# Kernel tuning notes

Measured on AMD Instinct MI355X. Metric: run time of the kernel, lower is better.

## Reference

```python
import jax, jax.numpy as jnp
import numpy as np

P = 100   # num_proxies
N = 1024  # num_samples
D = 512


def _edge_index():
    # complete bipartite proxy<->sample graph, both directions, plus self-loops
    # (PyG GATConv adds self-loops for all nodes by default)
    p = np.arange(P)
    s = np.arange(P, P + N)
    src_ps = np.repeat(p, N)   # proxy -> sample
    dst_ps = np.tile(s, P)
    loops = np.arange(P + N)
    src = np.concatenate([src_ps, dst_ps, loops]).astype(np.int32)
    dst = np.concatenate([dst_ps, src_ps, loops]).astype(np.int32)
    return jnp.asarray(src), jnp.asarray(dst)


def setup_inputs() -> dict:
    key = jax.random.key(0)
    ks = jax.random.split(key, 10)
    sc = 1.0 / np.sqrt(D)
    src, dst = _edge_index()
    return {
        "x": jax.random.normal(ks[0], (N, D), jnp.float32),
        "proxies": jax.random.normal(ks[1], (P, D), jnp.float32),
        "W1": jax.random.normal(ks[2], (D, D), jnp.float32) * sc,
        "a_src1": jax.random.normal(ks[3], (D,), jnp.float32) * sc,
        "a_dst1": jax.random.normal(ks[4], (D,), jnp.float32) * sc,
        "b1": jnp.zeros((D,), jnp.float32),
        "W2": jax.random.normal(ks[5], (D, D), jnp.float32) * sc,
        "a_src2": jax.random.normal(ks[6], (D,), jnp.float32) * sc,
        "a_dst2": jax.random.normal(ks[7], (D,), jnp.float32) * sc,
        "b2": jnp.zeros((D,), jnp.float32),
        "fc_w": jax.random.normal(ks[8], (D, 100), jnp.float32) * sc,
        "fc_b": jnp.zeros((100,), jnp.float32),
        "src": src,
        "dst": dst,
    }


def _gat_conv(x, src, dst, W, a_src, a_dst, b, n_nodes):
    # PyG GATConv, heads=1, concat=True, negative_slope=0.2
    h = x @ W                      # [n, D]
    l_src = h @ a_src              # [n]
    l_dst = h @ a_dst              # [n]
    e = jax.nn.leaky_relu(l_src[src] + l_dst[dst], 0.2)   # [E]
    # segment softmax over edges sharing the same destination
    e = e - jax.ops.segment_max(e, dst, num_segments=n_nodes)[dst]
    ex = jnp.exp(e)
    denom = jax.ops.segment_sum(ex, dst, num_segments=n_nodes)[dst]
    alpha = ex / denom             # [E]
    out = jax.ops.segment_sum(alpha[:, None] * h[src], dst, num_segments=n_nodes)
    return out + b


def reference(x, proxies, W1, a_src1, a_dst1, b1, W2, a_src2, a_dst2, b2, fc_w, fc_b, src, dst):
    n = P + N
    h = jnp.concatenate([proxies, x], axis=0)          # [P+N, D]
    h = jax.nn.relu(_gat_conv(h, src, dst, W1, a_src1, a_dst1, b1, n))
    # Dropout -> identity (eval)
    h = jax.nn.relu(_gat_conv(h, src, dst, W2, a_src2, a_dst2, b2, n))
    preds = h @ fc_w + fc_b                            # [P+N, 100]
    return preds[P:], h[P:]
```

## Files before the change

### kernel.cpp

```cpp
#include <hip/hip_runtime.h>

#define PP 100
#define NS 1024
#define NN 1124
#define DD 512
#define CC 100
#define NTHR 256

typedef _Float16 f16;
typedef _Float16 f16x8 __attribute__((ext_vector_type(8)));
typedef float    f32x4 __attribute__((ext_vector_type(4)));

__device__ __forceinline__ float lk(float v) { return v > 0.f ? v : 0.2f * v; }
__device__ __forceinline__ f16 hif(float v) { return (f16)v; }
__device__ __forceinline__ f16 lof(float v) { return (f16)(v - (float)((f16)v)); }

__device__ __forceinline__ void mgemm_core(
    const f16* __restrict__ Ah, const f16* __restrict__ Al,
    const f16* __restrict__ Bth, const f16* __restrict__ Btl,
    int K, int row0, int col0, f16* __restrict__ lds, f32x4 acc[2][2])
{
  const int t = threadIdx.x;
  const int lane = t & 63, w = t >> 6;
  const int wr = w >> 1, wc = w & 1;
  f16* Ash = lds;
  f16* Asl = lds + 2560;
  f16* Bsh = lds + 5120;
  f16* Bsl = lds + 7680;
  const int srow = t >> 2, su = t & 3;
  const size_t aoff = (size_t)(row0 + srow) * K + su * 8;
  const size_t boff = (size_t)(col0 + srow) * K + su * 8;
  const int lw = srow * 40 + su * 8;
  f32x4 pa0 = *(const f32x4*)(Ah + aoff);
  f32x4 pa1 = *(const f32x4*)(Al + aoff);
  f32x4 pb0 = *(const f32x4*)(Bth + boff);
  f32x4 pb1 = *(const f32x4*)(Btl + boff);
  const int fra = wr * 32 + (lane & 15);
  const int frb = wc * 32 + (lane & 15);
  const int fu  = (lane >> 4) * 8;
  for (int kt = 32; kt <= K; kt += 32) {
    *(f32x4*)(Ash + lw) = pa0;
    *(f32x4*)(Asl + lw) = pa1;
    *(f32x4*)(Bsh + lw) = pb0;
    *(f32x4*)(Bsl + lw) = pb1;
    __syncthreads();
    if (kt < K) {
      pa0 = *(const f32x4*)(Ah + aoff + kt);
      pa1 = *(const f32x4*)(Al + aoff + kt);
      pb0 = *(const f32x4*)(Bth + boff + kt);
      pb1 = *(const f32x4*)(Btl + boff + kt);
    }
    f16x8 ah[2], al[2], bh[2], bl[2];
#pragma unroll
    for (int m = 0; m < 2; ++m) {
      ah[m] = *(const f16x8*)(Ash + (fra + m * 16) * 40 + fu);
      al[m] = *(const f16x8*)(Asl + (fra + m * 16) * 40 + fu);
    }
#pragma unroll
    for (int n = 0; n < 2; ++n) {
      bh[n] = *(const f16x8*)(Bsh + (frb + n * 16) * 40 + fu);
      bl[n] = *(const f16x8*)(Bsl + (frb + n * 16) * 40 + fu);
    }
#pragma unroll
    for (int m = 0; m < 2; ++m)
#pragma unroll
      for (int n = 0; n < 2; ++n) {
        acc[m][n] = __builtin_amdgcn_mfma_f32_16x16x32_f16(ah[m], bh[n], acc[m][n], 0, 0, 0);
        acc[m][n] = __builtin_amdgcn_mfma_f32_16x16x32_f16(al[m], bh[n], acc[m][n], 0, 0, 0);
        acc[m][n] = __builtin_amdgcn_mfma_f32_16x16x32_f16(ah[m], bl[n], acc[m][n], 0, 0, 0);
      }
    __syncthreads();
  }
}


__device__ __forceinline__ void cvt_tile(
    const float* __restrict__ in, int R, int Cin,
    f16* __restrict__ oh, f16* __restrict__ ol, int ldo,
    int ti, int tj, f16 (*th)[72], f16 (*tl)[72])
{
  const int t = threadIdx.x;
#pragma unroll
  for (int p = 0; p < 4; ++p) {
    const int f = t + p * 256;
    const int i = f >> 4, j4 = (f & 15) * 4;
    const int gi = ti * 64 + i, gj = tj * 64 + j4;
    float4 v = make_float4(0.f, 0.f, 0.f, 0.f);
    if (gi < R && gj + 3 < Cin) v = *(const float4*)(in + (size_t)gi * Cin + gj);
    th[i][j4 + 0] = hif(v.x); tl[i][j4 + 0] = lof(v.x);
    th[i][j4 + 1] = hif(v.y); tl[i][j4 + 1] = lof(v.y);
    th[i][j4 + 2] = hif(v.z); tl[i][j4 + 2] = lof(v.z);
    th[i][j4 + 3] = hif(v.w); tl[i][j4 + 3] = lof(v.w);
  }
  __syncthreads();
#pragma unroll
  for (int p = 0; p < 2; ++p) {
    const int f = t + p * 256;
    const int j = f >> 3, i8 = (f & 7) * 8;
    f16x8 vh, vl;
#pragma unroll
    for (int e = 0; e < 8; ++e) { vh[e] = th[i8 + e][j]; vl[e] = tl[i8 + e][j]; }
    const size_t o = (size_t)(tj * 64 + j) * ldo + ti * 64 + i8;
    *(f16x8*)(oh + o) = vh;
    *(f16x8*)(ol + o) = vl;
  }
}

__global__ __launch_bounds__(NTHR) void prep_k(
    const float* __restrict__ x, const float* __restrict__ prox,
    const float* __restrict__ W1, const float* __restrict__ W2,
    const float* __restrict__ fcw,
    const float* __restrict__ as1, const float* __restrict__ ad1,
    const float* __restrict__ as2, const float* __restrict__ ad2,
    f16* xth, f16* xtl, f16* pth, f16* ptl,
    f16* W1th, f16* W1tl, f16* W2th, f16* W2tl, f16* fwth, f16* fwtl,
    float* v1s, float* v1d, float* v2s, float* v2d)
{
  __shared__ f16 th[64][72];
  __shared__ f16 tl[64][72];
  const int b = blockIdx.x;
  if (b < 64) {
    cvt_tile(W1, 512, 512, W1th, W1tl, 512, b >> 3, b & 7, th, tl);
  } else if (b < 128) {
    cvt_tile(W2, 512, 512, W2th, W2tl, 512, (b - 64) >> 3, (b - 64) & 7, th, tl);
  } else if (b < 256) {
    cvt_tile(x, NS, 512, xth, xtl, NS, (b - 128) >> 3, (b - 128) & 7, th, tl);
  } else if (b < 272) {
    cvt_tile(prox, PP, 512, pth, ptl, 128, (b - 256) >> 3, (b - 256) & 7, th, tl);
  } else if (b < 288) {
    cvt_tile(fcw, 512, CC, fwth, fwtl, 512, (b - 272) >> 1, (b - 272) & 1, th, tl);
  } else {
    const int wid  = (b - 288) * 4 + (threadIdx.x >> 6);
    const int lane = threadIdx.x & 63;
    const int r = wid & 511;
    const bool l1 = (wid < 512);
    const float* W = l1 ? W1 : W2;
    const float4* a4 = (const float4*)(l1 ? as1 : as2);
    const float4* b4 = (const float4*)(l1 ? ad1 : ad2);
    const float4* w4 = (const float4*)(W + (size_t)r * DD);
    float4 w0 = w4[lane], w1 = w4[lane + 64];
    float4 a0 = a4[lane], a1 = a4[lane + 64];
    float4 b0 = b4[lane], b1 = b4[lane + 64];
    float s1 = w0.x * a0.x + w0.y * a0.y + w0.z * a0.z + w0.w * a0.w
             + w1.x * a1.x + w1.y * a1.y + w1.z * a1.z + w1.w * a1.w;
    float s2 = w0.x * b0.x + w0.y * b0.y + w0.z * b0.z + w0.w * b0.w
             + w1.x * b1.x + w1.y * b1.y + w1.z * b1.z + w1.w * b1.w;
#pragma unroll
    for (int off = 32; off > 0; off >>= 1) {
      s1 += __shfl_down(s1, off);
      s2 += __shfl_down(s2, off);
    }
    if (lane == 0) {
      (l1 ? v1s : v2s)[r] = s1;
      (l1 ? v1d : v2d)[r] = s2;
    }
  }
}

__global__ __launch_bounds__(NTHR) void lvec_k(
    const float* __restrict__ A0, const float* __restrict__ A1, int split,
    const float* __restrict__ vs, const float* __restrict__ vd,
    float* __restrict__ ls, float* __restrict__ ld)
{
  const int r    = blockIdx.x * 4 + (threadIdx.x >> 6);
  const int lane = threadIdx.x & 63;
  if (r >= NN) return;
  const float* row = (r < split) ? A0 + (size_t)r * DD : A1 + (size_t)(r - split) * DD;
  const float4* r4 = (const float4*)row;
  const float4* s4 = (const float4*)vs;
  const float4* d4 = (const float4*)vd;
  float4 v0 = r4[lane], v1 = r4[lane + 64];
  float4 a0 = s4[lane], a1 = s4[lane + 64];
  float4 b0 = d4[lane], b1 = d4[lane + 64];
  float s1 = v0.x * a0.x + v0.y * a0.y + v0.z * a0.z + v0.w * a0.w
           + v1.x * a1.x + v1.y * a1.y + v1.z * a1.z + v1.w * a1.w;
  float s2 = v0.x * b0.x + v0.y * b0.y + v0.z * b0.z + v0.w * b0.w
           + v1.x * b1.x + v1.y * b1.y + v1.z * b1.z + v1.w * b1.w;
#pragma unroll
  for (int off = 32; off > 0; off >>= 1) {
    s1 += __shfl_down(s1, off);
    s2 += __shfl_down(s2, off);
  }
  if (lane == 0) { ls[r] = s1; ld[r] = s2; }
}

__global__ __launch_bounds__(NTHR) void alpha_k(
    const float* __restrict__ ls, const float* __restrict__ ld,
    f16* __restrict__ Esh, f16* __restrict__ Esl,
    float* __restrict__ esS, float* __restrict__ izS,
    f16* __restrict__ Eph, f16* __restrict__ Epl,
    float* __restrict__ esP, float* __restrict__ izP)
{
  const int t = threadIdx.x;
  if (blockIdx.x < 256) {
    const int lane = t & 63;
    const int i = blockIdx.x * 4 + (t >> 6);
    const float ldi = ld[PP + i];
    float e0 = lk(ls[lane] + ldi);
    float e1 = (lane < PP - 64) ? lk(ls[lane + 64] + ldi) : -1e30f;
    const float eself = lk(ls[PP + i] + ldi);
    float m = fmaxf(fmaxf(e0, e1), eself);
#pragma unroll
    for (int off = 1; off < 64; off <<= 1) m = fmaxf(m, __shfl_xor(m, off));
    float x0 = __expf(e0 - m);
    float x1 = (lane < PP - 64) ? __expf(e1 - m) : 0.f;
    float z = x0 + x1;
#pragma unroll
    for (int off = 1; off < 64; off <<= 1) z += __shfl_xor(z, off);
    Esh[(size_t)i * 128 + lane]      = hif(x0);
    Esl[(size_t)i * 128 + lane]      = lof(x0);
    Esh[(size_t)i * 128 + 64 + lane] = hif(x1);
    Esl[(size_t)i * 128 + 64 + lane] = lof(x1);
    if (lane == 0) {
      float xs = __expf(eself - m);
      esS[i] = xs;
      izS[i] = 1.f / (z + xs);
    }
  } else {
    const int i = blockIdx.x - 256;
    if (i >= PP) {
#pragma unroll
      for (int q = 0; q < 4; ++q) {
        Eph[(size_t)i * NS + t + q * 256] = (f16)0.f;
        Epl[(size_t)i * NS + t + q * 256] = (f16)0.f;
      }
      return;
    }
    __shared__ float red[4];
    const float ldi = ld[i];
    const float eself = lk(ls[i] + ldi);
    float e[4];
#pragma unroll
    for (int q = 0; q < 4; ++q) e[q] = lk(ls[PP + t + q * 256] + ldi);
    float m = fmaxf(fmaxf(fmaxf(e[0], e[1]), fmaxf(e[2], e[3])), eself);
#pragma unroll
    for (int off = 1; off < 64; off <<= 1) m = fmaxf(m, __shfl_xor(m, off));
    if ((t & 63) == 0) red[t >> 6] = m;
    __syncthreads();
    m = fmaxf(fmaxf(red[0], red[1]), fmaxf(red[2], red[3]));
    __syncthreads();
    float xq[4], z = 0.f;
#pragma unroll
    for (int q = 0; q < 4; ++q) { xq[q] = __expf(e[q] - m); z += xq[q]; }
#pragma unroll
    for (int off = 1; off < 64; off <<= 1) z += __shfl_xor(z, off);
    if ((t & 63) == 0) red[t >> 6] = z;
    __syncthreads();
#pragma unroll
    for (int q = 0; q < 4; ++q) {
      Eph[(size_t)i * NS + t + q * 256] = hif(xq[q]);
      Epl[(size_t)i * NS + t + q * 256] = lof(xq[q]);
    }
    if (t == 0) {
      float xs = __expf(eself - m);
      esP[i] = xs;
      izP[i] = 1.f / (red[0] + red[1] + red[2] + red[3] + xs);
    }
  }
}

__global__ __launch_bounds__(NTHR) void agg1_k(
    const f16* __restrict__ Es1h, const f16* __restrict__ Es1l,
    const f16* __restrict__ pth,  const f16* __restrict__ ptl,
    const f16* __restrict__ Eph,  const f16* __restrict__ Epl,
    const f16* __restrict__ xth,  const f16* __restrict__ xtl,
    const float* __restrict__ x, const float* __restrict__ prox,
    const float* __restrict__ esS, const float* __restrict__ izS,
    const float* __restrict__ esP, const float* __restrict__ izP,
    f16* __restrict__ M1h, f16* __restrict__ M1l)
{
  __shared__ __align__(16) f16 lds[10240];
  f32x4 acc[2][2] = {};
  const int t = threadIdx.x, lane = t & 63, w = t >> 6, wr = w >> 1, wc = w & 1;
  const int b = blockIdx.x;
  if (b < 128) {
    const int row0 = (b >> 3) * 64, col0 = (b & 7) * 64;
    mgemm_core(Es1h, Es1l, pth, ptl, 128, row0, col0, lds, acc);
#pragma unroll
    for (int m = 0; m < 2; ++m)
#pragma unroll
      for (int q = 0; q < 4; ++q) {
        const int r = row0 + wr * 32 + m * 16 + (lane >> 4) * 4 + q;
        const float e = esS[r], z = izS[r];
#pragma unroll
        for (int n = 0; n < 2; ++n) {
          const int c = col0 + wc * 32 + n * 16 + (lane & 15);
          const float v = (acc[m][n][q] + e * x[(size_t)r * DD + c]) * z;
          const size_t o = (size_t)(PP + r) * DD + c;
          M1h[o] = hif(v); M1l[o] = lof(v);
        }
      }
  } else {
    const int b2 = b - 128;
    const int row0 = (b2 >> 3) * 64, col0 = (b2 & 7) * 64;
    mgemm_core(Eph, Epl, xth, xtl, NS, row0, col0, lds, acc);
#pragma unroll
    for (int m = 0; m < 2; ++m)
#pragma unroll
      for (int q = 0; q < 4; ++q) {
        const int r = row0 + wr * 32 + m * 16 + (lane >> 4) * 4 + q;
        if (r < PP) {
          const float e = esP[r], z = izP[r];
#pragma unroll
          for (int n = 0; n < 2; ++n) {
            const int c = col0 + wc * 32 + n * 16 + (lane & 15);
            const float v = (acc[m][n][q] + e * prox[(size_t)r * DD + c]) * z;
            const size_t o = (size_t)r * DD + c;
            M1h[o] = hif(v); M1l[o] = lof(v);
          }
        }
      }
  }
}

__global__ __launch_bounds__(NTHR) void h1_k(
    const f16* __restrict__ M1h, const f16* __restrict__ M1l,
    const f16* __restrict__ W1th, const f16* __restrict__ W1tl,
    const float* __restrict__ b1, float* __restrict__ h1,
    f16* __restrict__ h1pth, f16* __restrict__ h1ptl)
{
  __shared__ __align__(16) f16 lds[10240];
  f32x4 acc[2][2] = {};
  const int t = threadIdx.x, lane = t & 63, w = t >> 6, wr = w >> 1, wc = w & 1;
  const int b = blockIdx.x;
  const int row0 = (b >> 3) * 64, col0 = (b & 7) * 64;
  mgemm_core(M1h, M1l, W1th, W1tl, DD, row0, col0, lds, acc);
#pragma unroll
  for (int m = 0; m < 2; ++m)
#pragma unroll
    for (int q = 0; q < 4; ++q) {
      const int r = row0 + wr * 32 + m * 16 + (lane >> 4) * 4 + q;
      if (r >= NN) continue;
#pragma unroll
      for (int n = 0; n < 2; ++n) {
        const int c = col0 + wc * 32 + n * 16 + (lane & 15);
        const float v = fmaxf(acc[m][n][q] + b1[c], 0.f);
        h1[(size_t)r * DD + c] = v;
        if (r < 128) {
          const size_t o = (size_t)c * 128 + r;
          f16 hh = (f16)0.f, ll = (f16)0.f;
          if (r < PP) { hh = hif(v); ll = lof(v); }
          h1pth[o] = hh; h1ptl[o] = ll;
        }
      }
    }
}

__global__ __launch_bounds__(NTHR) void agg2_k(
    const f16* __restrict__ Es2h, const f16* __restrict__ Es2l,
    const f16* __restrict__ h1pth, const f16* __restrict__ h1ptl,
    const float* __restrict__ h1,
    const float* __restrict__ esS, const float* __restrict__ izS,
    f16* __restrict__ M2h, f16* __restrict__ M2l)
{
  __shared__ __align__(16) f16 lds[10240];
  f32x4 acc[2][2] = {};
  const int t = threadIdx.x, lane = t & 63, w = t >> 6, wr = w >> 1, wc = w & 1;
  const int b = blockIdx.x;
  const int row0 = (b >> 3) * 64, col0 = (b & 7) * 64;
  mgemm_core(Es2h, Es2l, h1pth, h1ptl, 128, row0, col0, lds, acc);
#pragma unroll
  for (int m = 0; m < 2; ++m)
#pragma unroll
    for (int q = 0; q < 4; ++q) {
      const int r = row0 + wr * 32 + m * 16 + (lane >> 4) * 4 + q;
      const float e = esS[r], z = izS[r];
#pragma unroll
      for (int n = 0; n < 2; ++n) {
        const int c = col0 + wc * 32 + n * 16 + (lane & 15);
        const float v = (acc[m][n][q] + e * h1[(size_t)(PP + r) * DD + c]) * z;
        const size_t o = (size_t)r * DD + c;
        M2h[o] = hif(v); M2l[o] = lof(v);
      }
    }
}

__global__ __launch_bounds__(NTHR) void h2_k(
    const f16* __restrict__ M2h, const f16* __restrict__ M2l,
    const f16* __restrict__ W2th, const f16* __restrict__ W2tl,
    const float* __restrict__ b2, float* __restrict__ h2s,
    f16* __restrict__ h2h, f16* __restrict__ h2l)
{
  __shared__ __align__(16) f16 lds[10240];
  f32x4 acc[2][2] = {};
  const int t = threadIdx.x, lane = t & 63, w = t >> 6, wr = w >> 1, wc = w & 1;
  const int b = blockIdx.x;
  const int row0 = (b >> 3) * 64, col0 = (b & 7) * 64;
  mgemm_core(M2h, M2l, W2th, W2tl, DD, row0, col0, lds, acc);
#pragma unroll
  for (int m = 0; m < 2; ++m)
#pragma unroll
    for (int q = 0; q < 4; ++q) {
      const int r = row0 + wr * 32 + m * 16 + (lane >> 4) * 4 + q;
#pragma unroll
      for (int n = 0; n < 2; ++n) {
        const int c = col0 + wc * 32 + n * 16 + (lane & 15);
        const float v = fmaxf(acc[m][n][q] + b2[c], 0.f);
        const size_t o = (size_t)r * DD + c;
        h2s[o] = v;
        h2h[o] = hif(v); h2l[o] = lof(v);
      }
    }
}

__global__ __launch_bounds__(NTHR) void fc_k(
    const f16* __restrict__ h2h, const f16* __restrict__ h2l,
    const f16* __restrict__ fwth, const f16* __restrict__ fwtl,
    const float* __restrict__ fcb, float* __restrict__ out)
{
  __shared__ __align__(16) f16 lds[10240];
  f32x4 acc[2][2] = {};
  const int t = threadIdx.x, lane = t & 63, w = t >> 6, wr = w >> 1, wc = w & 1;
  const int b = blockIdx.x;
  const int row0 = (b >> 1) * 64, col0 = (b & 1) * 64;
  mgemm_core(h2h, h2l, fwth, fwtl, DD, row0, col0, lds, acc);
#pragma unroll
  for (int m = 0; m < 2; ++m)
#pragma unroll
    for (int q = 0; q < 4; ++q) {
      const int r = row0 + wr * 32 + m * 16 + (lane >> 4) * 4 + q;
#pragma unroll
      for (int n = 0; n < 2; ++n) {
        const int c = col0 + wc * 32 + n * 16 + (lane & 15);
        if (c < CC) out[(size_t)r * CC + c] = acc[m][n][q] + fcb[c];
      }
    }
}

extern "C" void kernel_launch(void* const* d_in, const int* in_sizes, int n_in,
                              void* d_out, int out_size, void* d_ws, size_t ws_size,
                              hipStream_t stream)
{
  const float* x    = (const float*)d_in[0];
  const float* prox = (const float*)d_in[1];
  const float* W1   = (const float*)d_in[2];
  const float* as1  = (const float*)d_in[3];
  const float* ad1  = (const float*)d_in[4];
  const float* b1   = (const float*)d_in[5];
  const float* W2   = (const float*)d_in[6];
  const float* as2  = (const float*)d_in[7];
  const float* ad2  = (const float*)d_in[8];
  const float* b2   = (const float*)d_in[9];
  const float* fcw  = (const float*)d_in[10];
  const float* fcb  = (const float*)d_in[11];
  float* out = (float*)d_out;

  float* F = (float*)d_ws;
  float* h1   = F; F += (size_t)NN * DD;
  float* ls1  = F; F += 1152;
  float* ld1  = F; F += 1152;
  float* ls2  = F; F += 1152;
  float* ld2  = F; F += 1152;
  float* v1s  = F; F += DD;
  float* v1d  = F; F += DD;
  float* v2s  = F; F += DD;
  float* v2d  = F; F += DD;
  float* esS1 = F; F += NS;
  float* izS1 = F; F += NS;
  float* esS2 = F; F += NS;
  float* izS2 = F; F += NS;
  float* esP  = F; F += 128;
  float* izP  = F; F += 128;
  f16* H = (f16*)F;
  f16* M1h  = H; H += (size_t)1152 * DD;
  f16* M1l  = H; H += (size_t)1152 * DD;
  f16* M2h  = H; H += (size_t)NS * DD;
  f16* M2l  = H; H += (size_t)NS * DD;
  f16* Es1h = H; H += (size_t)NS * 128;
  f16* Es1l = H; H += (size_t)NS * 128;
  f16* Es2h = H; H += (size_t)NS * 128;
  f16* Es2l = H; H += (size_t)NS * 128;
  f16* Eph  = H; H += (size_t)128 * NS;
  f16* Epl  = H; H += (size_t)128 * NS;
  f16* xth  = H; H += (size_t)DD * NS;
  f16* xtl  = H; H += (size_t)DD * NS;
  f16* pth  = H; H += (size_t)DD * 128;
  f16* ptl  = H; H += (size_t)DD * 128;
  f16* W1th = H; H += (size_t)DD * DD;
  f16* W1tl = H; H += (size_t)DD * DD;
  f16* W2th = H; H += (size_t)DD * DD;
  f16* W2tl = H; H += (size_t)DD * DD;
  f16* fwth = H; H += (size_t)128 * DD;
  f16* fwtl = H; H += (size_t)128 * DD;
  f16* h2h  = H; H += (size_t)NS * DD;
  f16* h2l  = H; H += (size_t)NS * DD;
  f16* h1pth = H; H += (size_t)DD * 128;
  f16* h1ptl = H; H += (size_t)DD * 128;
  float* h2s = out + (size_t)NS * CC;

  dim3 blk(NTHR);
  prep_k<<<dim3(544), blk, 0, stream>>>(x, prox, W1, W2, fcw, as1, ad1, as2, ad2,
      xth, xtl, pth, ptl, W1th, W1tl, W2th, W2tl, fwth, fwtl,
      v1s, v1d, v2s, v2d);
  lvec_k<<<dim3(281), blk, 0, stream>>>(prox, x, PP, v1s, v1d, ls1, ld1);
  alpha_k<<<dim3(256 + 128), blk, 0, stream>>>(ls1, ld1, Es1h, Es1l, esS1, izS1,
                                               Eph, Epl, esP, izP);
  agg1_k<<<dim3(144), blk, 0, stream>>>(Es1h, Es1l, pth, ptl, Eph, Epl, xth, xtl,
                                        x, prox, esS1, izS1, esP, izP, M1h, M1l);
  h1_k<<<dim3(144), blk, 0, stream>>>(M1h, M1l, W1th, W1tl, b1, h1, h1pth, h1ptl);
  lvec_k<<<dim3(281), blk, 0, stream>>>(h1, h1, NN, v2s, v2d, ls2, ld2);
  alpha_k<<<dim3(256), blk, 0, stream>>>(ls2, ld2, Es2h, Es2l, esS2, izS2,
                                         Eph, Epl, esP, izP);
  agg2_k<<<dim3(128), blk, 0, stream>>>(Es2h, Es2l, h1pth, h1ptl, h1,
                                        esS2, izS2, M2h, M2l);
  h2_k<<<dim3(128), blk, 0, stream>>>(M2h, M2l, W2th, W2tl, b2, h2s, h2h, h2l);
  fc_k<<<dim3(32), blk, 0, stream>>>(h2h, h2l, fwth, fwtl, fcb, out);
}
```

Measured before the change: 158.9 us.

## Fuse all stages into one cooperative persistent kernel with grid syncs

Result: slower. 419.1 us (+163.8%).

```diff
diff --git a/kernel.cpp b/kernel.cpp
--- a/kernel.cpp
+++ b/kernel.cpp
@@ -1,4 +1,6 @@
 #include <hip/hip_runtime.h>
+#include <hip/hip_cooperative_groups.h>
+namespace cg = cooperative_groups;
 
 #define PP 100
 #define NS 1024
@@ -14,6 +16,15 @@
 __device__ __forceinline__ float lk(float v) { return v > 0.f ? v : 0.2f * v; }
 __device__ __forceinline__ f16 hif(float v) { return (f16)v; }
 __device__ __forceinline__ f16 lof(float v) { return (f16)(v - (float)((f16)v)); }
+
+struct FA {
+  const float *x, *prox, *W1, *as1, *ad1, *b1, *W2, *as2, *ad2, *b2, *fcw, *fcb;
+  float *out, *h1, *ls1, *ld1, *ls2, *ld2, *v1s, *v1d, *v2s, *v2d;
+  float *esS1, *izS1, *esS2, *izS2, *esP, *izP, *h2s;
+  f16 *M1h, *M1l, *M2h, *M2l, *Es1h, *Es1l, *Es2h, *Es2l, *Eph, *Epl;
+  f16 *xth, *xtl, *pth, *ptl, *W1th, *W1tl, *W2th, *W2tl, *fwth, *fwtl;
+  f16 *h2h, *h2l, *h1pth, *h1ptl;
+};
 
 __device__ __forceinline__ void mgemm_core(
     const f16* __restrict__ Ah, const f16* __restrict__ Al,
@@ -106,37 +117,27 @@
   }
 }
 
-__global__ __launch_bounds__(NTHR) void prep_k(
-    const float* __restrict__ x, const float* __restrict__ prox,
-    const float* __restrict__ W1, const float* __restrict__ W2,
-    const float* __restrict__ fcw,
-    const float* __restrict__ as1, const float* __restrict__ ad1,
-    const float* __restrict__ as2, const float* __restrict__ ad2,
-    f16* xth, f16* xtl, f16* pth, f16* ptl,
-    f16* W1th, f16* W1tl, f16* W2th, f16* W2tl, f16* fwth, f16* fwtl,
-    float* v1s, float* v1d, float* v2s, float* v2d)
-{
-  __shared__ f16 th[64][72];
-  __shared__ f16 tl[64][72];
-  const int b = blockIdx.x;
-  if (b < 64) {
-    cvt_tile(W1, 512, 512, W1th, W1tl, 512, b >> 3, b & 7, th, tl);
-  } else if (b < 128) {
-    cvt_tile(W2, 512, 512, W2th, W2tl, 512, (b - 64) >> 3, (b - 64) & 7, th, tl);
-  } else if (b < 256) {
-    cvt_tile(x, NS, 512, xth, xtl, NS, (b - 128) >> 3, (b - 128) & 7, th, tl);
-  } else if (b < 272) {
-    cvt_tile(prox, PP, 512, pth, ptl, 128, (b - 256) >> 3, (b - 256) & 7, th, tl);
-  } else if (b < 288) {
-    cvt_tile(fcw, 512, CC, fwth, fwtl, 512, (b - 272) >> 1, (b - 272) & 1, th, tl);
+
+__device__ void dv_prep(int u, const FA& a, f16 (*th)[72], f16 (*tl)[72])
+{
+  if (u < 64) {
+    cvt_tile(a.W1, 512, 512, a.W1th, a.W1tl, 512, u >> 3, u & 7, th, tl);
+  } else if (u < 128) {
+    cvt_tile(a.W2, 512, 512, a.W2th, a.W2tl, 512, (u - 64) >> 3, (u - 64) & 7, th, tl);
+  } else if (u < 256) {
+    cvt_tile(a.x, NS, 512, a.xth, a.xtl, NS, (u - 128) >> 3, (u - 128) & 7, th, tl);
+  } else if (u < 272) {
+    cvt_tile(a.prox, PP, 512, a.pth, a.ptl, 128, (u - 256) >> 3, (u - 256) & 7, th, tl);
+  } else if (u < 288) {
+    cvt_tile(a.fcw, 512, CC, a.fwth, a.fwtl, 512, (u - 272) >> 1, (u - 272) & 1, th, tl);
   } else {
-    const int wid  = (b - 288) * 4 + (threadIdx.x >> 6);
+    const int wid  = (u - 288) * 4 + (threadIdx.x >> 6);
     const int lane = threadIdx.x & 63;
     const int r = wid & 511;
     const bool l1 = (wid < 512);
-    const float* W = l1 ? W1 : W2;
-    const float4* a4 = (const float4*)(l1 ? as1 : as2);
-    const float4* b4 = (const float4*)(l1 ? ad1 : ad2);
+    const float* W = l1 ? a.W1 : a.W2;
+    const float4* a4 = (const float4*)(l1 ? a.as1 : a.as2);
+    const float4* b4 = (const float4*)(l1 ? a.ad1 : a.ad2);
     const float4* w4 = (const float4*)(W + (size_t)r * DD);
     float4 w0 = w4[lane], w1 = w4[lane + 64];
     float4 a0 = a4[lane], a1 = a4[lane + 64];
@@ -151,18 +152,16 @@
       s2 += __shfl_down(s2, off);
     }
     if (lane == 0) {
-      (l1 ? v1s : v2s)[r] = s1;
-      (l1 ? v1d : v2d)[r] = s2;
-    }
-  }
-}
-
-__global__ __launch_bounds__(NTHR) void lvec_k(
-    const float* __restrict__ A0, const float* __restrict__ A1, int split,
-    const float* __restrict__ vs, const float* __restrict__ vd,
-    float* __restrict__ ls, float* __restrict__ ld)
-{
-  const int r    = blockIdx.x * 4 + (threadIdx.x >> 6);
+      (l1 ? a.v1s : a.v2s)[r] = s1;
+      (l1 ? a.v1d : a.v2d)[r] = s2;
+    }
+  }
+}
+
+__device__ void dv_lvec(int u, const float* A0, const float* A1, int split,
+                        const float* vs, const float* vd, float* ls, float* ld)
+{
+  const int r    = u * 4 + (threadIdx.x >> 6);
   const int lane = threadIdx.x & 63;
   if (r >= NN) return;
   const float* row = (r < split) ? A0 + (size_t)r * DD : A1 + (size_t)(r - split) * DD;
@@ -184,17 +183,14 @@
   if (lane == 0) { ls[r] = s1; ld[r] = s2; }
 }
 
-__global__ __launch_bounds__(NTHR) void alpha_k(
-    const float* __restrict__ ls, const float* __restrict__ ld,
-    f16* __restrict__ Esh, f16* __restrict__ Esl,
-    float* __restrict__ esS, float* __restrict__ izS,
-    f16* __restrict__ Eph, f16* __restrict__ Epl,
-    float* __restrict__ esP, float* __restrict__ izP)
+__device__ void dv_alpha(int u, const float* ls, const float* ld,
+                         f16* Esh, f16* Esl, float* esS, float* izS,
+                         f16* Eph, f16* Epl, float* esP, float* izP, float* red)
 {
   const int t = threadIdx.x;
-  if (blockIdx.x < 256) {
+  if (u < 256) {
     const int lane = t & 63;
-    const int i = blockIdx.x * 4 + (t >> 6);
+    const int i = u * 4 + (t >> 6);
     const float ldi = ld[PP + i];
     float e0 = lk(ls[lane] + ldi);
     float e1 = (lane < PP - 64) ? lk(ls[lane + 64] + ldi) : -1e30f;
@@ -217,7 +213,7 @@
       izS[i] = 1.f / (z + xs);
     }
   } else {
-    const int i = blockIdx.x - 256;
+    const int i = u - 256;
     if (i >= PP) {
 #pragma unroll
       for (int q = 0; q < 4; ++q) {
@@ -226,7 +222,6 @@
       }
       return;
     }
-    __shared__ float red[4];
     const float ldi = ld[i];
     const float eself = lk(ls[i] + ldi);
     float e[4];
@@ -259,72 +254,56 @@
   }
 }
 
-__global__ __launch_bounds__(NTHR) void agg1_k(
-    const f16* __restrict__ Es1h, const f16* __restrict__ Es1l,
-    const f16* __restrict__ pth,  const f16* __restrict__ ptl,
-    const f16* __restrict__ Eph,  const f16* __restrict__ Epl,
-    const f16* __restrict__ xth,  const f16* __restrict__ xtl,
-    const float* __restrict__ x, const float* __restrict__ prox,
-    const float* __restrict__ esS, const float* __restrict__ izS,
-    const float* __restrict__ esP, const float* __restrict__ izP,
-    f16* __restrict__ M1h, f16* __restrict__ M1l)
-{
-  __shared__ __align__(16) f16 lds[10240];
+__device__ void dv_agg1(int u, const FA& a, f16* lds)
+{
   f32x4 acc[2][2] = {};
   const int t = threadIdx.x, lane = t & 63, w = t >> 6, wr = w >> 1, wc = w & 1;
-  const int b = blockIdx.x;
-  if (b < 128) {
-    const int row0 = (b >> 3) * 64, col0 = (b & 7) * 64;
-    mgemm_core(Es1h, Es1l, pth, ptl, 128, row0, col0, lds, acc);
+  if (u < 128) {
+    const int row0 = (u >> 3) * 64, col0 = (u & 7) * 64;
+    mgemm_core(a.Es1h, a.Es1l, a.pth, a.ptl, 128, row0, col0, lds, acc);
 #pragma unroll
     for (int m = 0; m < 2; ++m)
 #pragma unroll
       for (int q = 0; q < 4; ++q) {
         const int r = row0 + wr * 32 + m * 16 + (lane >> 4) * 4 + q;
-        const float e = esS[r], z = izS[r];
+        const float e = a.esS1[r], z = a.izS1[r];
 #pragma unroll
         for (int n = 0; n < 2; ++n) {
           const int c = col0 + wc * 32 + n * 16 + (lane & 15);
-          const float v = (acc[m][n][q] + e * x[(size_t)r * DD + c]) * z;
+          const float v = (acc[m][n][q] + e * a.x[(size_t)r * DD + c]) * z;
           const size_t o = (size_t)(PP + r) * DD + c;
-          M1h[o] = hif(v); M1l[o] = lof(v);
+          a.M1h[o] = hif(v); a.M1l[o] = lof(v);
         }
       }
   } else {
-    const int b2 = b - 128;
+    const int b2 = u - 128;
     const int row0 = (b2 >> 3) * 64, col0 = (b2 & 7) * 64;
-    mgemm_core(Eph, Epl, xth, xtl, NS, row0, col0, lds, acc);
+    mgemm_core(a.Eph, a.Epl, a.xth, a.xtl, NS, row0, col0, lds, acc);
 #pragma unroll
     for (int m = 0; m < 2; ++m)
 #pragma unroll
       for (int q = 0; q < 4; ++q) {
         const int r = row0 + wr * 32 + m * 16 + (lane >> 4) * 4 + q;
         if (r < PP) {
-          const float e = esP[r], z = izP[r];
+          const float e = a.esP[r], z = a.izP[r];
 #pragma unroll
           for (int n = 0; n < 2; ++n) {
             const int c = col0 + wc * 32 + n * 16 + (lane & 15);
-            const float v = (acc[m][n][q] + e * prox[(size_t)r * DD + c]) * z;
+            const float v = (acc[m][n][q] + e * a.prox[(size_t)r * DD + c]) * z;
             const size_t o = (size_t)r * DD + c;
-            M1h[o] = hif(v); M1l[o] = lof(v);
+            a.M1h[o] = hif(v); a.M1l[o] = lof(v);
           }
         }
       }
   }
 }
 
-__global__ __launch_bounds__(NTHR) void h1_k(
-    const f16* __restrict__ M1h, const f16* __restrict__ M1l,
-    const f16* __restrict__ W1th, const f16* __restrict__ W1tl,
-    const float* __restrict__ b1, float* __restrict__ h1,
-    f16* __restrict__ h1pth, f16* __restrict__ h1ptl)
-{
-  __shared__ __align__(16) f16 lds[10240];
+__device__ void dv_h1(int u, const FA& a, f16* lds)
+{
   f32x4 acc[2][2] = {};
   const int t = threadIdx.x, lane = t & 63, w = t >> 6, wr = w >> 1, wc = w & 1;
-  const int b = blockIdx.x;
-  const int row0 = (b >> 3) * 64, col0 = (b & 7) * 64;
-  mgemm_core(M1h, M1l, W1th, W1tl, DD, row0, col0, lds, acc);
+  const int row0 = (u >> 3) * 64, col0 = (u & 7) * 64;
+  mgemm_core(a.M1h, a.M1l, a.W1th, a.W1tl, DD, row0, col0, lds, acc);
 #pragma unroll
   for (int m = 0; m < 2; ++m)
 #pragma unroll
@@ -334,59 +313,46 @@
 #pragma unroll
       for (int n = 0; n < 2; ++n) {
         const int c = col0 + wc * 32 + n * 16 + (lane & 15);
-        const float v = fmaxf(acc[m][n][q] + b1[c], 0.f);
-        h1[(size_t)r * DD + c] = v;
+        const float v = fmaxf(acc[m][n][q] + a.b1[c], 0.f);
+        a.h1[(size_t)r * DD + c] = v;
         if (r < 128) {
           const size_t o = (size_t)c * 128 + r;
           f16 hh = (f16)0.f, ll = (f16)0.f;
           if (r < PP) { hh = hif(v); ll = lof(v); }
-          h1pth[o] = hh; h1ptl[o] = ll;
+          a.h1pth[o] = hh; a.h1ptl[o] = ll;
         }
       }
     }
 }
 
-__global__ __launch_bounds__(NTHR) void agg2_k(
-    const f16* __restrict__ Es2h, const f16* __restrict__ Es2l,
-    const f16* __restrict__ h1pth, const f16* __restrict__ h1ptl,
-    const float* __restrict__ h1,
-    const float* __restrict__ esS, const float* __restrict__ izS,
-    f16* __restrict__ M2h, f16* __restrict__ M2l)
-{
-  __shared__ __align__(16) f16 lds[10240];
+__device__ void dv_agg2(int u, const FA& a, f16* lds)
+{
   f32x4 acc[2][2] = {};
   const int t = threadIdx.x, lane = t & 63, w = t >> 6, wr = w >> 1, wc = w & 1;
-  const int b = blockIdx.x;
-  const int row0 = (b >> 3) * 64, col0 = (b & 7) * 64;
-  mgemm_core(Es2h, Es2l, h1pth, h1ptl, 128, row0, col0, lds, acc);
+  const int row0 = (u >> 3) * 64, col0 = (u & 7) * 64;
+  mgemm_core(a.Es2h, a.Es2l, a.h1pth, a.h1ptl, 128, row0, col0, lds, acc);
 #pragma unroll
   for (int m = 0; m < 2; ++m)
 #pragma unroll
     for (int q = 0; q < 4; ++q) {
       const int r = row0 + wr * 32 + m * 16 + (lane >> 4) * 4 + q;
-      const float e = esS[r], z = izS[r];
+      const float e = a.esS2[r], z = a.izS2[r];
 #pragma unroll
       for (int n = 0; n < 2; ++n) {
         const int c = col0 + wc * 32 + n * 16 + (lane & 15);
-        const float v = (acc[m][n][q] + e * h1[(size_t)(PP + r) * DD + c]) * z;
+        const float v = (acc[m][n][q] + e * a.h1[(size_t)(PP + r) * DD + c]) * z;
         const size_t o = (size_t)r * DD + c;
-        M2h[o] = hif(v); M2l[o] = lof(v);
-      }
-    }
-}
-
-__global__ __launch_bounds__(NTHR) void h2_k(
-    const f16* __restrict__ M2h, const f16* __restrict__ M2l,
-    const f16* __restrict__ W2th, const f16* __restrict__ W2tl,
-    const float* __restrict__ b2, float* __restrict__ h2s,
-    f16* __restrict__ h2h, f16* __restrict__ h2l)
-{
-  __shared__ __align__(16) f16 lds[10240];
+        a.M2h[o] = hif(v); a.M2l[o] = lof(v);
+      }
+    }
+}
+
+__device__ void dv_h2(int u, const FA& a, f16* lds)
+{
   f32x4 acc[2][2] = {};
   const int t = threadIdx.x, lane = t & 63, w = t >> 6, wr = w >> 1, wc = w & 1;
-  const int b = blockIdx.x;
-  const int row0 = (b >> 3) * 64, col0 = (b & 7) * 64;
-  mgemm_core(M2h, M2l, W2th, W2tl, DD, row0, col0, lds, acc);
+  const int row0 = (u >> 3) * 64, col0 = (u & 7) * 64;
+  mgemm_core(a.M2h, a.M2l, a.W2th, a.W2tl, DD, row0, col0, lds, acc);
 #pragma unroll
   for (int m = 0; m < 2; ++m)
 #pragma unroll
@@ -395,25 +361,20 @@
 #pragma unroll
       for (int n = 0; n < 2; ++n) {
         const int c = col0 + wc * 32 + n * 16 + (lane & 15);
-        const float v = fmaxf(acc[m][n][q] + b2[c], 0.f);
+        const float v = fmaxf(acc[m][n][q] + a.b2[c], 0.f);
         const size_t o = (size_t)r * DD + c;
-        h2s[o] = v;
-        h2h[o] = hif(v); h2l[o] = lof(v);
-      }
-    }
-}
-
-__global__ __launch_bounds__(NTHR) void fc_k(
-    const f16* __restrict__ h2h, const f16* __restrict__ h2l,
-    const f16* __restrict__ fwth, const f16* __restrict__ fwtl,
-    const float* __restrict__ fcb, float* __restrict__ out)
-{
-  __shared__ __align__(16) f16 lds[10240];
+        a.h2s[o] = v;
+        a.h2h[o] = hif(v); a.h2l[o] = lof(v);
+      }
+    }
+}
+
+__device__ void dv_fc(int u, const FA& a, f16* lds)
+{
   f32x4 acc[2][2] = {};
   const int t = threadIdx.x, lane = t & 63, w = t >> 6, wr = w >> 1, wc = w & 1;
-  const int b = blockIdx.x;
-  const int row0 = (b >> 1) * 64, col0 = (b & 1) * 64;
-  mgemm_core(h2h, h2l, fwth, fwtl, DD, row0, col0, lds, acc);
+  const int row0 = (u >> 1) * 64, col0 = (u & 1) * 64;
+  mgemm_core(a.h2h, a.h2l, a.fwth, a.fwtl, DD, row0, col0, lds, acc);
 #pragma unroll
   for (int m = 0; m < 2; ++m)
 #pragma unroll
@@ -422,87 +383,173 @@
 #pragma unroll
       for (int n = 0; n < 2; ++n) {
         const int c = col0 + wc * 32 + n * 16 + (lane & 15);
-        if (c < CC) out[(size_t)r * CC + c] = acc[m][n][q] + fcb[c];
-      }
-    }
+        if (c < CC) a.out[(size_t)r * CC + c] = acc[m][n][q] + a.fcb[c];
+      }
+    }
+}
+
+__global__ __launch_bounds__(NTHR) void fused_k(FA a)
+{
+  cg::grid_group g = cg::this_grid();
+  __shared__ __align__(16) f16 lds[10240];
+  __shared__ float red[4];
+  f16 (*th)[72] = (f16(*)[72])lds;
+  f16 (*tl)[72] = (f16(*)[72])(lds + 4608);
+
+  for (int u = blockIdx.x; u < 544; u += gridDim.x) {
+    dv_prep(u, a, th, tl);
+    __syncthreads();
+  }
+  g.sync();
+  for (int u = blockIdx.x; u < 281; u += gridDim.x)
+    dv_lvec(u, a.prox, a.x, PP, a.v1s, a.v1d, a.ls1, a.ld1);
+  g.sync();
+  for (int u = blockIdx.x; u < 384; u += gridDim.x) {
+    dv_alpha(u, a.ls1, a.ld1, a.Es1h, a.Es1l, a.esS1, a.izS1,
+             a.Eph, a.Epl, a.esP, a.izP, red);
+    __syncthreads();
+  }
+  g.sync();
+  for (int u = blockIdx.x; u < 144; u += gridDim.x)
+    dv_agg1(u, a, lds);
+  g.sync();
+  for (int u = blockIdx.x; u < 144; u += gridDim.x)
+    dv_h1(u, a, lds);
+  g.sync();
+  for (int u = blockIdx.x; u < 281; u += gridDim.x)
+    dv_lvec(u, a.h1, a.h1, NN, a.v2s, a.v2d, a.ls2, a.ld2);
+  g.sync();
+  for (int u = blockIdx.x; u < 256; u += gridDim.x) {
+    dv_alpha(u, a.ls2, a.ld2, a.Es2h, a.Es2l, a.esS2, a.izS2,
+             a.Eph, a.Epl, a.esP, a.izP, red);
+    __syncthreads();
+  }
+  g.sync();
+  for (int u = blockIdx.x; u < 128; u += gridDim.x)
+    dv_agg2(u, a, lds);
+  g.sync();
+  for (int u = blockIdx.x; u < 128; u += gridDim.x)
+    dv_h2(u, a, lds);
+  g.sync();
+  for (int u = blockIdx.x; u < 32; u += gridDim.x)
+    dv_fc(u, a, lds);
+}
+
+__global__ __launch_bounds__(NTHR) void prep_k(FA a) {
+  __shared__ f16 th[64][72];
+  __shared__ f16 tl[64][72];
+  dv_prep(blockIdx.x, a, th, tl);
+}
+__global__ __launch_bounds__(NTHR) void lvec_k(FA a, int layer) {
+  if (layer == 1) dv_lvec(blockIdx.x, a.prox, a.x, PP, a.v1s, a.v1d, a.ls1, a.ld1);
+  else            dv_lvec(blockIdx.x, a.h1, a.h1, NN, a.v2s, a.v2d, a.ls2, a.ld2);
+}
+__global__ __launch_bounds__(NTHR) void alpha_k(FA a, int layer) {
+  __shared__ float red[4];
+  if (layer == 1)
+    dv_alpha(blockIdx.x, a.ls1, a.ld1, a.Es1h, a.Es1l, a.esS1, a.izS1,
+             a.Eph, a.Epl, a.esP, a.izP, red);
+  else
+    dv_alpha(blockIdx.x, a.ls2, a.ld2, a.Es2h, a.Es2l, a.esS2, a.izS2,
+             a.Eph, a.Epl, a.esP, a.izP, red);
+}
+__global__ __launch_bounds__(NTHR) void agg1_k(FA a) {
+  __shared__ __align__(16) f16 lds[10240];
+  dv_agg1(blockIdx.x, a, lds);
+}
+__global__ __launch_bounds__(NTHR) void h1_k(FA a) {
+  __shared__ __align__(16) f16 lds[10240];
+  dv_h1(blockIdx.x, a, lds);
+}
+__global__ __launch_bounds__(NTHR) void agg2_k(FA a) {
+  __shared__ __align__(16) f16 lds[10240];
+  dv_agg2(blockIdx.x, a, lds);
+}
+__global__ __launch_bounds__(NTHR) void h2_k(FA a) {
+  __shared__ __align__(16) f16 lds[10240];
+  dv_h2(blockIdx.x, a, lds);
+}
+__global__ __launch_bounds__(NTHR) void fc_k(FA a) {
+  __shared__ __align__(16) f16 lds[10240];
+  dv_fc(blockIdx.x, a, lds);
 }
 
 extern "C" void kernel_launch(void* const* d_in, const int* in_sizes, int n_in,
                               void* d_out, int out_size, void* d_ws, size_t ws_size,
                               hipStream_t stream)
 {
-  const float* x    = (const float*)d_in[0];
-  const float* prox = (const float*)d_in[1];
-  const float* W1   = (const float*)d_in[2];
-  const float* as1  = (const float*)d_in[3];
-  const float* ad1  = (const float*)d_in[4];
-  const float* b1   = (const float*)d_in[5];
-  const float* W2   = (const float*)d_in[6];
-  const float* as2  = (const float*)d_in[7];
-  const float* ad2  = (const float*)d_in[8];
-  const float* b2   = (const float*)d_in[9];
-  const float* fcw  = (const float*)d_in[10];
-  const float* fcb  = (const float*)d_in[11];
-  float* out = (float*)d_out;
+  FA a;
+  a.x    = (const float*)d_in[0];
+  a.prox = (const float*)d_in[1];
+  a.W1   = (const float*)d_in[2];
+  a.as1  = (const float*)d_in[3];
+  a.ad1  = (const float*)d_in[4];
+  a.b1   = (const float*)d_in[5];
+  a.W2   = (const float*)d_in[6];
+  a.as2  = (const float*)d_in[7];
+  a.ad2  = (const float*)d_in[8];
+  a.b2   = (const float*)d_in[9];
+  a.fcw  = (const float*)d_in[10];
+  a.fcb  = (const float*)d_in[11];
+  a.out  = (float*)d_out;
 
   float* F = (float*)d_ws;
-  float* h1   = F; F += (size_t)NN * DD;
-  float* ls1  = F; F += 1152;
-  float* ld1  = F; F += 1152;
-  float* ls2  = F; F += 1152;
-  float* ld2  = F; F += 1152;
-  float* v1s  = F; F += DD;
-  float* v1d  = F; F += DD;
-  float* v2s  = F; F += DD;
-  float* v2d  = F; F += DD;
-  float* esS1 = F; F += NS;
-  float* izS1 = F; F += NS;
-  float* esS2 = F; F += NS;
-  float* izS2 = F; F += NS;
-  float* esP  = F; F += 128;
-  float* izP  = F; F += 128;
+  a.h1   = F; F += (size_t)NN * DD;
+  a.ls1  = F; F += 1152;
+  a.ld1  = F; F += 1152;
+  a.ls2  = F; F += 1152;
+  a.ld2  = F; F += 1152;
+  a.v1s  = F; F += DD;
+  a.v1d  = F; F += DD;
+  a.v2s  = F; F += DD;
+  a.v2d  = F; F += DD;
+  a.esS1 = F; F += NS;
+  a.izS1 = F; F += NS;
+  a.esS2 = F; F += NS;
+  a.izS2 = F; F += NS;
+  a.esP  = F; F += 128;
+  a.izP  = F; F += 128;
   f16* H = (f16*)F;
-  f16* M1h  = H; H += (size_t)1152 * DD;
-  f16* M1l  = H; H += (size_t)1152 * DD;
-  f16* M2h  = H; H += (size_t)NS * DD;
-  f16* M2l  = H; H += (size_t)NS * DD;
-  f16* Es1h = H; H += (size_t)NS * 128;
-  f16* Es1l = H; H += (size_t)NS * 128;
-  f16* Es2h = H; H += (size_t)NS * 128;
-  f16* Es2l = H; H += (size_t)NS * 128;
-  f16* Eph  = H; H += (size_t)128 * NS;
-  f16* Epl  = H; H += (size_t)128 * NS;
-  f16* xth  = H; H += (size_t)DD * NS;
-  f16* xtl  = H; H += (size_t)DD * NS;
-  f16* pth  = H; H += (size_t)DD * 128;
-  f16* ptl  = H; H += (size_t)DD * 128;
-  f16* W1th = H; H += (size_t)DD * DD;
-  f16* W1tl = H; H += (size_t)DD * DD;
-  f16* W2th = H; H += (size_t)DD * DD;
-  f16* W2tl = H; H += (size_t)DD * DD;
-  f16* fwth = H; H += (size_t)128 * DD;
-  f16* fwtl = H; H += (size_t)128 * DD;
-  f16* h2h  = H; H += (size_t)NS * DD;
-  f16* h2l  = H; H += (size_t)NS * DD;
-  f16* h1pth = H; H += (size_t)DD * 128;
-  f16* h1ptl = H; H += (size_t)DD * 128;
-  float* h2s = out + (size_t)NS * CC;
+  a.M1h  = H; H += (size_t)1152 * DD;
+  a.M1l  = H; H += (size_t)1152 * DD;
+  a.M2h  = H; H += (size_t)NS * DD;
+  a.M2l  = H; H += (size_t)NS * DD;
+  a.Es1h = H; H += (size_t)NS * 128;
+  a.Es1l = H; H += (size_t)NS * 128;
+  a.Es2h = H; H += (size_t)NS * 128;
+  a.Es2l = H; H += (size_t)NS * 128;
+  a.Eph  = H; H += (size_t)128 * NS;
+  a.Epl  = H; H += (size_t)128 * NS;
+  a.xth  = H; H += (size_t)DD * NS;
+  a.xtl  = H; H += (size_t)DD * NS;
+  a.pth  = H; H += (size_t)DD * 128;
+  a.ptl  = H; H += (size_t)DD * 128;
+  a.W1th = H; H += (size_t)DD * DD;
+  a.W1tl = H; H += (size_t)DD * DD;
+  a.W2th = H; H += (size_t)DD * DD;
+  a.W2tl = H; H += (size_t)DD * DD;
+  a.fwth = H; H += (size_t)128 * DD;
+  a.fwtl = H; H += (size_t)128 * DD;
+  a.h2h  = H; H += (size_t)NS * DD;
+  a.h2l  = H; H += (size_t)NS * DD;
+  a.h1pth = H; H += (size_t)DD * 128;
+  a.h1ptl = H; H += (size_t)DD * 128;
+  a.h2s  = a.out + (size_t)NS * CC;
 
   dim3 blk(NTHR);
-  prep_k<<<dim3(544), blk, 0, stream>>>(x, prox, W1, W2, fcw, as1, ad1, as2, ad2,
-      xth, xtl, pth, ptl, W1th, W1tl, W2th, W2tl, fwth, fwtl,
-      v1s, v1d, v2s, v2d);
-  lvec_k<<<dim3(281), blk, 0, stream>>>(prox, x, PP, v1s, v1d, ls1, ld1);
-  alpha_k<<<dim3(256 + 128), blk, 0, stream>>>(ls1, ld1, Es1h, Es1l, esS1, izS1,
-                                               Eph, Epl, esP, izP);
-  agg1_k<<<dim3(144), blk, 0, stream>>>(Es1h, Es1l, pth, ptl, Eph, Epl, xth, xtl,
-                                        x, prox, esS1, izS1, esP, izP, M1h, M1l);
-  h1_k<<<dim3(144), blk, 0, stream>>>(M1h, M1l, W1th, W1tl, b1, h1, h1pth, h1ptl);
-  lvec_k<<<dim3(281), blk, 0, stream>>>(h1, h1, NN, v2s, v2d, ls2, ld2);
-  alpha_k<<<dim3(256), blk, 0, stream>>>(ls2, ld2, Es2h, Es2l, esS2, izS2,
-                                         Eph, Epl, esP, izP);
-  agg2_k<<<dim3(128), blk, 0, stream>>>(Es2h, Es2l, h1pth, h1ptl, h1,
-                                        esS2, izS2, M2h, M2l);
-  h2_k<<<dim3(128), blk, 0, stream>>>(M2h, M2l, W2th, W2tl, b2, h2s, h2h, h2l);
-  fc_k<<<dim3(32), blk, 0, stream>>>(h2h, h2l, fwth, fwtl, fcb, out);
-}
+  void* params[] = { (void*)&a };
+  hipError_t err = hipLaunchCooperativeKernel(
+      (const void*)fused_k, dim3(256), blk, params, 0, stream);
+  if (err != hipSuccess) {
+    prep_k <<<dim3(544), blk, 0, stream>>>(a);
+    lvec_k <<<dim3(281), blk, 0, stream>>>(a, 1);
+    alpha_k<<<dim3(384), blk, 0, stream>>>(a, 1);
+    agg1_k <<<dim3(144), blk, 0, stream>>>(a);
+    h1_k   <<<dim3(144), blk, 0, stream>>>(a);
+    lvec_k <<<dim3(281), blk, 0, stream>>>(a, 2);
+    alpha_k<<<dim3(256), blk, 0, stream>>>(a, 2);
+    agg2_k <<<dim3(128), blk, 0, stream>>>(a);
+    h2_k   <<<dim3(128), blk, 0, stream>>>(a);
+    fc_k   <<<dim3(32),  blk, 0, stream>>>(a);
+  }
+}
```
